# Kernel optimization log

Measured on AMD Instinct MI355X. Metric: run time of the kernel, lower is better.

Reference implementation:

```python
import jax, jax.numpy as jnp
import numpy as np

BB_SCALE_TYPE = 'MinMax'  # init kwarg; one of MinMax/Min/Max


def _unproject_all(depth_map, intrinsics):
    # depth_map: [H, W]; returns per-pixel 3D points [H, W, 3]
    H, W = depth_map.shape
    fx, fy, cx, cy = intrinsics[0], intrinsics[1], intrinsics[2], intrinsics[3]
    xs = jnp.arange(W, dtype=depth_map.dtype)[None, :]   # x_d (column)
    ys = jnp.arange(H, dtype=depth_map.dtype)[:, None]   # y_d (row)
    x3 = (xs - cx) * depth_map / fx
    y3 = (ys - cy) * depth_map / fy
    return jnp.stack([x3, y3, depth_map], axis=-1)  # [H, W, 3]


def _scale_to_unit(points, mask):
    # points: [H, W, 3]; mask: [H, W] bool. Masked bbox min/max then norm.
    m = mask[..., None]
    big = jnp.asarray(jnp.finfo(points.dtype).max, points.dtype)
    max_b = jnp.max(jnp.where(m, points, -big), axis=(0, 1))  # [3]
    min_b = jnp.min(jnp.where(m, points, big), axis=(0, 1))   # [3]
    if BB_SCALE_TYPE == 'MinMax':
        return jnp.linalg.norm(max_b - min_b)
    if BB_SCALE_TYPE == 'Min':
        return jnp.linalg.norm(min_b)
    return jnp.linalg.norm(max_b)


def setup_inputs() -> dict:
    key = jax.random.key(0)
    k1, k2, k3 = jax.random.split(key, 3)
    H, W = 2048, 2048
    depth_estimations = jax.random.uniform(k1, (1, 1, H, W), jnp.float32) * 10.0 + 0.1
    sparse_depths = jax.random.uniform(k2, (1, 1, H, W), jnp.float32) * 10.0 + 0.1
    sparse_depth_masks = jax.random.randint(k3, (1, 1, H, W), 0, 2, jnp.int32)
    intrinsics = jnp.array([500.0, 500.0, 1024.0, 1024.0], jnp.float32)  # fx, fy, cx, cy
    return {
        'depth_estimations': depth_estimations,
        'sparse_depths': sparse_depths,
        'sparse_depth_masks': sparse_depth_masks,
        'intrinsics': intrinsics,
    }


def reference(depth_estimations, sparse_depths, sparse_depth_masks, intrinsics):
    mask = sparse_depth_masks[0, 0] != 0  # [H, W]
    pts_sparse = _unproject_all(sparse_depths[0, 0], intrinsics)
    pts_dense = _unproject_all(depth_estimations[0, 0], intrinsics)
    scale_sparse = _scale_to_unit(pts_sparse, mask)
    scale_dense = _scale_to_unit(pts_dense, mask)
    rescaled_depth = (scale_sparse / scale_dense) * depth_estimations
    std = jnp.asarray(1.0, depth_estimations.dtype)
    return (rescaled_depth, std)
```

## Files before the change

kernel.cpp:

```cpp
#include <hip/hip_runtime.h>
#include <float.h>

static constexpr int H    = 2048;
static constexpr int Wd   = 2048;
static constexpr int NPIX = H * Wd;
static constexpr int BT   = 256;
static constexpr int N4   = NPIX / 4;

static constexpr int NB1   = 1024;
static constexpr int ITER1 = N4 / (NB1 * BT);
static constexpr int NB2   = 2048;
static constexpr int ITER2 = N4 / (NB2 * BT);


__global__ __launch_bounds__(BT) void reduce_bbox_kernel(
    const float* __restrict__ dense,
    const float* __restrict__ sparse,
    const int*   __restrict__ mask,
    const float* __restrict__ intr,
    float* __restrict__ ws)
{
    const float cx = intr[2], cy = intr[3];
    const float qnan = __uint_as_float(0x7FC00000u);

    const float4* d4 = (const float4*)dense;
    const float4* s4 = (const float4*)sparse;
    const int4*   m4 = (const int4*)mask;

    const int tid = blockIdx.x * BT + threadIdx.x;

    float loc[12];
#pragma unroll
    for (int s = 0; s < 12; ++s) loc[s] = ((s % 6) < 3) ? FLT_MAX : -FLT_MAX;

    int4   mv[ITER1];
    float4 sv[ITER1];
    float4 dv[ITER1];
#pragma unroll
    for (int k = 0; k < ITER1; ++k) {
        const int i = tid + k * (NB1 * BT);
        mv[k] = m4[i];
        sv[k] = s4[i];
        dv[k] = d4[i];
    }

#pragma unroll
    for (int k = 0; k < ITER1; ++k) {
        const int i = tid + k * (NB1 * BT);
        const int base = i << 2;
        const float yc = (float)(base >> 11) - cy;
        const float xf = (float)(base & 2047);
        const int   mm[4] = { mv[k].x, mv[k].y, mv[k].z, mv[k].w };
        const float dd[4] = { dv[k].x, dv[k].y, dv[k].z, dv[k].w };
        const float ss[4] = { sv[k].x, sv[k].y, sv[k].z, sv[k].w };
#pragma unroll
        for (int j = 0; j < 4; ++j) {
            float sd = (mm[j] != 0) ? ss[j] : qnan;
            float de = (mm[j] != 0) ? dd[j] : qnan;
            float xc = xf + (float)j - cx;
            float spx = xc * sd;
            float spy = yc * sd;
            float dpx = xc * de;
            float dpy = yc * de;
            loc[0] = fminf(loc[0], spx); loc[3]  = fmaxf(loc[3],  spx);
            loc[1] = fminf(loc[1], spy); loc[4]  = fmaxf(loc[4],  spy);
            loc[2] = fminf(loc[2], sd ); loc[5]  = fmaxf(loc[5],  sd );
            loc[6] = fminf(loc[6], dpx); loc[9]  = fmaxf(loc[9],  dpx);
            loc[7] = fminf(loc[7], dpy); loc[10] = fmaxf(loc[10], dpy);
            loc[8] = fminf(loc[8], de ); loc[11] = fmaxf(loc[11], de );
        }
    }

#pragma unroll
    for (int off = 32; off > 0; off >>= 1) {
#pragma unroll
        for (int s = 0; s < 12; ++s) {
            float o = __shfl_xor(loc[s], off, 64);
            loc[s] = ((s % 6) < 3) ? fminf(loc[s], o) : fmaxf(loc[s], o);
        }
    }

    __shared__ float red[4][12];
    const int lane = threadIdx.x & 63;
    const int wid  = threadIdx.x >> 6;
    if (lane == 0) {
#pragma unroll
        for (int s = 0; s < 12; ++s) red[wid][s] = loc[s];
    }
    __syncthreads();

    if (threadIdx.x < 12) {
        const int s = threadIdx.x;
        const bool is_min = (s % 6) < 3;
        float v = red[0][s];
#pragma unroll
        for (int w = 1; w < 4; ++w)
            v = is_min ? fminf(v, red[w][s]) : fmaxf(v, red[w][s]);
        ws[s * NB1 + blockIdx.x] = v;
    }
}

__global__ __launch_bounds__(BT) void finalize_scale_kernel(
    const float* __restrict__ dense,
    const float* __restrict__ intr,
    const float* __restrict__ ws,
    float* __restrict__ out)
{
    const int tid = blockIdx.x * BT + threadIdx.x;
    const float4* d4 = (const float4*)dense;

    float4 v0 = d4[tid];
    float4 v1 = d4[tid + NB2 * BT];

    static_assert(NB1 / 4 == BT, "one float4 per thread per slot");
    const float4* p4 = (const float4*)ws;
    float loc[12];
#pragma unroll
    for (int s = 0; s < 12; ++s) {
        float4 p = p4[s * BT + threadIdx.x];
        if ((s % 6) < 3)
            loc[s] = fminf(fminf(p.x, p.y), fminf(p.z, p.w));
        else
            loc[s] = fmaxf(fmaxf(p.x, p.y), fmaxf(p.z, p.w));
    }

#pragma unroll
    for (int off = 32; off > 0; off >>= 1) {
#pragma unroll
        for (int s = 0; s < 12; ++s) {
            float o = __shfl_xor(loc[s], off, 64);
            loc[s] = ((s % 6) < 3) ? fminf(loc[s], o) : fmaxf(loc[s], o);
        }
    }

    __shared__ float red[4][12];
    __shared__ float ratio_sh;
    const int lane = threadIdx.x & 63;
    const int wid  = threadIdx.x >> 6;
    if (lane == 0) {
#pragma unroll
        for (int s = 0; s < 12; ++s) red[wid][s] = loc[s];
    }
    __syncthreads();

    if (threadIdx.x == 0) {
        float fin[12];
#pragma unroll
        for (int s = 0; s < 12; ++s) {
            const bool is_min = (s % 6) < 3;
            float v = red[0][s];
#pragma unroll
            for (int w = 1; w < 4; ++w)
                v = is_min ? fminf(v, red[w][s]) : fmaxf(v, red[w][s]);
            fin[s] = v;
        }
        const float inv_fx = 1.0f / intr[0], inv_fy = 1.0f / intr[1];
        float sx = (fin[3]  - fin[0]) * inv_fx;
        float sy = (fin[4]  - fin[1]) * inv_fy;
        float sz =  fin[5]  - fin[2];
        float dx = (fin[9]  - fin[6]) * inv_fx;
        float dy = (fin[10] - fin[7]) * inv_fy;
        float dz =  fin[11] - fin[8];
        ratio_sh = sqrtf(sx*sx + sy*sy + sz*sz) / sqrtf(dx*dx + dy*dy + dz*dz);
    }
    __syncthreads();

    const float r = ratio_sh;
    float4* o4 = (float4*)out;
    o4[tid]            = make_float4(v0.x * r, v0.y * r, v0.z * r, v0.w * r);
    o4[tid + NB2 * BT] = make_float4(v1.x * r, v1.y * r, v1.z * r, v1.w * r);
    if (blockIdx.x == 0 && threadIdx.x == 0) out[NPIX] = 1.0f;
}

extern "C" void kernel_launch(void* const* d_in, const int* in_sizes, int n_in,
                              void* d_out, int out_size, void* d_ws, size_t ws_size,
                              hipStream_t stream) {
    const float* dense  = (const float*)d_in[0];
    const float* sparse = (const float*)d_in[1];
    const int*   mask   = (const int*)d_in[2];
    const float* intr   = (const float*)d_in[3];

    float* out  = (float*)d_out;
    float* ws_f = (float*)d_ws;

    reduce_bbox_kernel<<<NB1, BT, 0, stream>>>(dense, sparse, mask, intr, ws_f);
    finalize_scale_kernel<<<NB2, BT, 0, stream>>>(dense, intr, ws_f, out);
}
```

Baseline: 26.26 us.

## Finalize bbox reduction in last block via atomic counter, doubling reduce grid

The final cross-block min/max reduction and ratio computation move out of the scale kernel into the last-arriving block of the reduce kernel, which it detects with an atomic ticket counter. The scale kernel then reads only a single precomputed ratio instead of re-reducing 12×NB1 partials in every block. The reduce grid doubles to 2048 blocks with an occupancy hint, and output stores become nontemporal. A memset launch is added to reset the counter each call, and the last block's serial tail adds latency to the reduce kernel.

Result: slower. 75.27 us (+186.6%).

```diff
diff --git a/kernel.cpp b/kernel.cpp
--- a/kernel.cpp
+++ b/kernel.cpp
@@ -7,19 +7,24 @@
 static constexpr int BT   = 256;
 static constexpr int N4   = NPIX / 4;
 
-static constexpr int NB1   = 1024;
+static constexpr int NB1   = 2048;
 static constexpr int ITER1 = N4 / (NB1 * BT);
 static constexpr int NB2   = 2048;
 static constexpr int ITER2 = N4 / (NB2 * BT);
 
-
-__global__ __launch_bounds__(BT) void reduce_bbox_kernel(
+typedef float f32x4 __attribute__((ext_vector_type(4)));
+
+
+__global__ __launch_bounds__(BT, 8) void reduce_bbox_kernel(
     const float* __restrict__ dense,
     const float* __restrict__ sparse,
     const int*   __restrict__ mask,
     const float* __restrict__ intr,
-    float* __restrict__ ws)
+    unsigned int* __restrict__ ws_u)
 {
+    float* partials = (float*)(ws_u + 4);
+    float* ratio_p  = partials + 12 * NB1;
+
     const float cx = intr[2], cy = intr[3];
     const float qnan = __uint_as_float(0x7FC00000u);
 
@@ -81,6 +86,7 @@
     }
 
     __shared__ float red[4][12];
+    __shared__ unsigned int last_sh;
     const int lane = threadIdx.x & 63;
     const int wid  = threadIdx.x >> 6;
     if (lane == 0) {
@@ -96,50 +102,47 @@
 #pragma unroll
         for (int w = 1; w < 4; ++w)
             v = is_min ? fminf(v, red[w][s]) : fmaxf(v, red[w][s]);
-        ws[s * NB1 + blockIdx.x] = v;
-    }
-}
-
-__global__ __launch_bounds__(BT) void finalize_scale_kernel(
-    const float* __restrict__ dense,
-    const float* __restrict__ intr,
-    const float* __restrict__ ws,
-    float* __restrict__ out)
-{
-    const int tid = blockIdx.x * BT + threadIdx.x;
-    const float4* d4 = (const float4*)dense;
-
-    float4 v0 = d4[tid];
-    float4 v1 = d4[tid + NB2 * BT];
-
-    static_assert(NB1 / 4 == BT, "one float4 per thread per slot");
-    const float4* p4 = (const float4*)ws;
-    float loc[12];
+        __hip_atomic_store(&partials[s * NB1 + blockIdx.x], v,
+                           __ATOMIC_RELAXED, __HIP_MEMORY_SCOPE_AGENT);
+    }
+    __syncthreads();
+
+    if (threadIdx.x == 0) {
+        unsigned int old = __hip_atomic_fetch_add(&ws_u[0], 1u,
+                               __ATOMIC_ACQ_REL, __HIP_MEMORY_SCOPE_AGENT);
+        last_sh = (old == (unsigned)(NB1 - 1)) ? 1u : 0u;
+    }
+    __syncthreads();
+
+    if (!last_sh) return;
+
+    __builtin_amdgcn_fence(__ATOMIC_ACQUIRE, "agent");
+
+    static_assert(NB1 / 4 == 2 * BT, "two float4 per thread per slot");
+    const float4* p4 = (const float4*)partials;
+    float loc2[12];
 #pragma unroll
     for (int s = 0; s < 12; ++s) {
-        float4 p = p4[s * BT + threadIdx.x];
+        float4 a = p4[s * (NB1 / 4) + threadIdx.x];
+        float4 b = p4[s * (NB1 / 4) + BT + threadIdx.x];
         if ((s % 6) < 3)
-            loc[s] = fminf(fminf(p.x, p.y), fminf(p.z, p.w));
+            loc2[s] = fminf(fminf(fminf(a.x, a.y), fminf(a.z, a.w)),
+                            fminf(fminf(b.x, b.y), fminf(b.z, b.w)));
         else
-            loc[s] = fmaxf(fmaxf(p.x, p.y), fmaxf(p.z, p.w));
-    }
-
+            loc2[s] = fmaxf(fmaxf(fmaxf(a.x, a.y), fmaxf(a.z, a.w)),
+                            fmaxf(fmaxf(b.x, b.y), fmaxf(b.z, b.w)));
+    }
 #pragma unroll
     for (int off = 32; off > 0; off >>= 1) {
 #pragma unroll
         for (int s = 0; s < 12; ++s) {
-            float o = __shfl_xor(loc[s], off, 64);
-            loc[s] = ((s % 6) < 3) ? fminf(loc[s], o) : fmaxf(loc[s], o);
-        }
-    }
-
-    __shared__ float red[4][12];
-    __shared__ float ratio_sh;
-    const int lane = threadIdx.x & 63;
-    const int wid  = threadIdx.x >> 6;
+            float o = __shfl_xor(loc2[s], off, 64);
+            loc2[s] = ((s % 6) < 3) ? fminf(loc2[s], o) : fmaxf(loc2[s], o);
+        }
+    }
     if (lane == 0) {
 #pragma unroll
-        for (int s = 0; s < 12; ++s) red[wid][s] = loc[s];
+        for (int s = 0; s < 12; ++s) red[wid][s] = loc2[s];
     }
     __syncthreads();
 
@@ -161,14 +164,37 @@
         float dx = (fin[9]  - fin[6]) * inv_fx;
         float dy = (fin[10] - fin[7]) * inv_fy;
         float dz =  fin[11] - fin[8];
-        ratio_sh = sqrtf(sx*sx + sy*sy + sz*sz) / sqrtf(dx*dx + dy*dy + dz*dz);
-    }
-    __syncthreads();
-
-    const float r = ratio_sh;
-    float4* o4 = (float4*)out;
-    o4[tid]            = make_float4(v0.x * r, v0.y * r, v0.z * r, v0.w * r);
-    o4[tid + NB2 * BT] = make_float4(v1.x * r, v1.y * r, v1.z * r, v1.w * r);
+        float ratio = sqrtf(sx*sx + sy*sy + sz*sz) /
+                      sqrtf(dx*dx + dy*dy + dz*dz);
+        __hip_atomic_store(ratio_p, ratio,
+                           __ATOMIC_RELEASE, __HIP_MEMORY_SCOPE_AGENT);
+    }
+}
+
+__global__ __launch_bounds__(BT) void scale_kernel(
+    const float* __restrict__ dense,
+    const float* __restrict__ ratio_p,
+    float* __restrict__ out)
+{
+    const int tid = blockIdx.x * BT + threadIdx.x;
+    const f32x4* d4 = (const f32x4*)dense;
+
+    f32x4 v0 = d4[tid];
+    f32x4 v1 = d4[tid + NB2 * BT];
+
+    __shared__ float rs;
+    if (threadIdx.x == 0) {
+        rs = __hip_atomic_load(ratio_p, __ATOMIC_RELAXED,
+                               __HIP_MEMORY_SCOPE_AGENT);
+    }
+    __syncthreads();
+    const float r = rs;
+
+    f32x4* o4 = (f32x4*)out;
+    f32x4 r0 = v0 * r;
+    f32x4 r1 = v1 * r;
+    __builtin_nontemporal_store(r0, &o4[tid]);
+    __builtin_nontemporal_store(r1, &o4[tid + NB2 * BT]);
     if (blockIdx.x == 0 && threadIdx.x == 0) out[NPIX] = 1.0f;
 }
 
@@ -180,9 +206,11 @@
     const int*   mask   = (const int*)d_in[2];
     const float* intr   = (const float*)d_in[3];
 
-    float* out  = (float*)d_out;
-    float* ws_f = (float*)d_ws;
-
-    reduce_bbox_kernel<<<NB1, BT, 0, stream>>>(dense, sparse, mask, intr, ws_f);
-    finalize_scale_kernel<<<NB2, BT, 0, stream>>>(dense, intr, ws_f, out);
+    float*        out   = (float*)d_out;
+    unsigned int* ws_u  = (unsigned int*)d_ws;
+    float*        ratio = (float*)(ws_u + 4) + 12 * NB1;
+
+    (void)hipMemsetAsync((void*)ws_u, 0, sizeof(unsigned int), stream);
+    reduce_bbox_kernel<<<NB1, BT, 0, stream>>>(dense, sparse, mask, intr, ws_u);
+    scale_kernel<<<NB2, BT, 0, stream>>>(dense, ratio, out);
 }
```

## Split finalize into single-block reduce plus streaming scale kernel, double reduce grid

Applied to the files above, without the earlier changes.

The cross-block bbox reduction now runs once in a one-block kernel that writes the ratio to workspace. Previously all 2048 scale blocks each re-reduced the whole partial array. The reduce grid doubles to 2048 blocks, and the scale kernel now does only load, multiply and nontemporal store. This removes redundant per-block reduction work. The cost is a third kernel launch and a serialized single-block step.

Measured after the change: 23.90 us (median of 2 runs). 1.1x faster.

```diff
diff --git a/kernel.cpp b/kernel.cpp
--- a/kernel.cpp
+++ b/kernel.cpp
@@ -7,10 +7,12 @@
 static constexpr int BT   = 256;
 static constexpr int N4   = NPIX / 4;
 
-static constexpr int NB1   = 1024;
+static constexpr int NB1   = 2048;
 static constexpr int ITER1 = N4 / (NB1 * BT);
 static constexpr int NB2   = 2048;
 static constexpr int ITER2 = N4 / (NB2 * BT);
+
+typedef float f32x4 __attribute__((ext_vector_type(4)));
 
 
 __global__ __launch_bounds__(BT) void reduce_bbox_kernel(
@@ -100,28 +102,25 @@
     }
 }
 
-__global__ __launch_bounds__(BT) void finalize_scale_kernel(
-    const float* __restrict__ dense,
+__global__ __launch_bounds__(BT) void finalize_kernel(
+    const float* __restrict__ ws,
     const float* __restrict__ intr,
-    const float* __restrict__ ws,
+    float* __restrict__ ratio_p,
     float* __restrict__ out)
 {
-    const int tid = blockIdx.x * BT + threadIdx.x;
-    const float4* d4 = (const float4*)dense;
-
-    float4 v0 = d4[tid];
-    float4 v1 = d4[tid + NB2 * BT];
-
-    static_assert(NB1 / 4 == BT, "one float4 per thread per slot");
+    static_assert(NB1 / 4 == 2 * BT, "two float4 per thread per slot");
     const float4* p4 = (const float4*)ws;
     float loc[12];
 #pragma unroll
     for (int s = 0; s < 12; ++s) {
-        float4 p = p4[s * BT + threadIdx.x];
+        float4 a = p4[s * (NB1 / 4) + threadIdx.x];
+        float4 b = p4[s * (NB1 / 4) + BT + threadIdx.x];
         if ((s % 6) < 3)
-            loc[s] = fminf(fminf(p.x, p.y), fminf(p.z, p.w));
+            loc[s] = fminf(fminf(fminf(a.x, a.y), fminf(a.z, a.w)),
+                           fminf(fminf(b.x, b.y), fminf(b.z, b.w)));
         else
-            loc[s] = fmaxf(fmaxf(p.x, p.y), fmaxf(p.z, p.w));
+            loc[s] = fmaxf(fmaxf(fmaxf(a.x, a.y), fmaxf(a.z, a.w)),
+                           fmaxf(fmaxf(b.x, b.y), fmaxf(b.z, b.w)));
     }
 
 #pragma unroll
@@ -134,7 +133,6 @@
     }
 
     __shared__ float red[4][12];
-    __shared__ float ratio_sh;
     const int lane = threadIdx.x & 63;
     const int wid  = threadIdx.x >> 6;
     if (lane == 0) {
@@ -161,15 +159,33 @@
         float dx = (fin[9]  - fin[6]) * inv_fx;
         float dy = (fin[10] - fin[7]) * inv_fy;
         float dz =  fin[11] - fin[8];
-        ratio_sh = sqrtf(sx*sx + sy*sy + sz*sz) / sqrtf(dx*dx + dy*dy + dz*dz);
-    }
+        ratio_p[0] = sqrtf(sx*sx + sy*sy + sz*sz) /
+                     sqrtf(dx*dx + dy*dy + dz*dz);
+        out[NPIX] = 1.0f;
+    }
+}
+
+__global__ __launch_bounds__(BT) void scale_kernel(
+    const float* __restrict__ dense,
+    const float* __restrict__ ratio_p,
+    float* __restrict__ out)
+{
+    const int tid = blockIdx.x * BT + threadIdx.x;
+    const f32x4* d4 = (const f32x4*)dense;
+
+    f32x4 v0 = d4[tid];
+    f32x4 v1 = d4[tid + NB2 * BT];
+
+    __shared__ float rs;
+    if (threadIdx.x == 0) rs = ratio_p[0];
     __syncthreads();
-
-    const float r = ratio_sh;
-    float4* o4 = (float4*)out;
-    o4[tid]            = make_float4(v0.x * r, v0.y * r, v0.z * r, v0.w * r);
-    o4[tid + NB2 * BT] = make_float4(v1.x * r, v1.y * r, v1.z * r, v1.w * r);
-    if (blockIdx.x == 0 && threadIdx.x == 0) out[NPIX] = 1.0f;
+    const float r = rs;
+
+    f32x4* o4 = (f32x4*)out;
+    f32x4 r0 = v0 * r;
+    f32x4 r1 = v1 * r;
+    __builtin_nontemporal_store(r0, &o4[tid]);
+    __builtin_nontemporal_store(r1, &o4[tid + NB2 * BT]);
 }
 
 extern "C" void kernel_launch(void* const* d_in, const int* in_sizes, int n_in,
@@ -180,9 +196,11 @@
     const int*   mask   = (const int*)d_in[2];
     const float* intr   = (const float*)d_in[3];
 
-    float* out  = (float*)d_out;
-    float* ws_f = (float*)d_ws;
+    float* out   = (float*)d_out;
+    float* ws_f  = (float*)d_ws;
+    float* ratio = ws_f + 12 * NB1;
 
     reduce_bbox_kernel<<<NB1, BT, 0, stream>>>(dense, sparse, mask, intr, ws_f);
-    finalize_scale_kernel<<<NB2, BT, 0, stream>>>(dense, intr, ws_f, out);
-}
+    finalize_kernel<<<1, BT, 0, stream>>>(ws_f, intr, ratio, out);
+    scale_kernel<<<NB2, BT, 0, stream>>>(dense, ratio, out);
+}
```
